# Optimization experiments

Measured on AMD Instinct MI355X. Metric: run time of the kernel, lower is better.

Reference implementation:

```python
import jax, jax.numpy as jnp
import numpy as np

# ---- maxflat pyramid filters (pfilters('maxflat')) ----
def _maxflat_filters():
    sqrt2 = np.sqrt(2.0)
    M1 = M2 = 1.0 / sqrt2
    k1 = 1.0 - sqrt2
    k2 = k3 = M1
    h_half = np.array([0.25 * k2 * k3, 0.5 * k2, 1.0 + 0.5 * k2 * k3]) * M1
    h = np.concatenate([h_half, h_half[:-1][::-1]]) * sqrt2          # len 5
    g_half = np.array([-0.125 * k1 * k2 * k3,
                       0.25 * k1 * k2,
                       -0.5 * k1 - 0.5 * k3 - 0.375 * k1 * k2 * k3,
                       1.0 + 0.5 * k1 * k2]) * M2
    g = np.concatenate([g_half, g_half[:-1][::-1]]) * sqrt2          # len 7
    return h.astype(np.float32), g.astype(np.float32)

# highpass from g, as in wfb2dec: h1 = -g * (-1)**(arange(1,L+1)-c)
def _wfb_filters():
    h, g = _maxflat_filters()
    len_h1 = len(g)                      # 7 (odd)
    c = int(np.floor((len_h1 + 1.0) / 2.0))   # 4
    h1 = (-g * (-1.0) ** (np.arange(1, len_h1 + 1) - c)).astype(np.float32)
    ext_h0 = int(np.floor(len(h) / 2.0))      # 2
    ext_h1 = len_h1 - c + 1                   # 4
    return h, h1, ext_h0, ext_h1

# periodic row filtering along last axis (torch rowfiltering: periodic pad +
# cross-correlation, which F.conv2d / lax conv both compute without flip)
def rowfilt(x, f, ext1):
    L = f.shape[0]
    ext2 = L - ext1 - 1
    W = x.shape[-1]
    xe = jnp.concatenate([x[..., -ext1:], x, x[..., :ext2]], axis=-1)
    y = f[0] * xe[..., 0:W]
    for k in range(1, L):                 # tiny fixed tap loop, fuses fine
        y = y + f[k] * xe[..., k:k + W]
    return y

def colfilt(x, f, ext1):
    return jnp.swapaxes(rowfilt(jnp.swapaxes(x, -1, -2), f, ext1), -1, -2)


def setup_inputs() -> dict:
    key = jax.random.key(0)
    x = jax.random.normal(key, (8, 3, 1024, 1024), dtype=jnp.float32)
    return {"x": x}


def reference(x):
    # Pycontourlet.batch_multi_channel_pdfbdec with pfilt='maxflat',
    # nlevs=[0] -> wfb2dec path: one level of separable wavelet FB with
    # periodic extension; returns [xLL, [xLH, xHL, xHH]] (stacked here).
    h_np, h1_np, e0, e1 = _wfb_filters()
    h = jnp.asarray(h_np)
    h1 = jnp.asarray(h1_np)

    x_L = rowfilt(x, h, e0)[..., ::2]          # [B,C,H,W/2]
    x_H = rowfilt(x, h1, e1)[..., ::2]

    x_LL = colfilt(x_L, h, e0)[..., ::2, :]    # [B,C,H/2,W/2]
    x_LH = colfilt(x_L, h1, e1)[..., ::2, :]
    x_HL = colfilt(x_H, h, e0)[..., ::2, :]
    x_HH = colfilt(x_H, h1, e1)[..., ::2, :]

    return jnp.stack([x_LL, x_LH, x_HL, x_HH])  # [4,B,C,H/2,W/2]
```

## Files before the change

kernel.cpp:

```cpp
#include <hip/hip_runtime.h>


constexpr int H = 1024, W = 1024;
constexpr int NIMG = 24;
constexpr int HOUT = 512, WOUT = 512;
constexpr int TO = 32;
constexpr int TI = 2 * TO + 6;

__global__ __launch_bounds__(256)
void wfb_kernel(const float* __restrict__ x, float* __restrict__ out) {
    __shared__ float s_in[TI][TI + 2];
    __shared__ float s_L[TI][TO + 1];
    __shared__ float s_H[TI][TO + 1];

    const float h0c[5] = {0.125f, 0.35355339059327373f, 1.25f,
                          0.35355339059327373f, 0.125f};
    const float h1c[7] = {0.025888347648318447f,  0.07322330470336313f,
                          -0.06878156646177083f, -0.8535533905932737f,
                          -0.06878156646177083f,  0.07322330470336313f,
                          0.025888347648318447f};

    const int tid = threadIdx.x;
    const int img = blockIdx.z;
    const int r0 = blockIdx.y * TO;
    const int c0 = blockIdx.x * TO;
    const float* __restrict__ xin = x + (size_t)img * H * W;

    const int rbase = 2 * r0 - 4;
    const int cbase = 2 * c0 - 4;
    for (int idx = tid; idx < TI * TI; idx += 256) {
        int r = idx / TI;
        int c = idx - r * TI;
        int gr = (rbase + r) & (H - 1);
        int gc = (cbase + c) & (W - 1);
        s_in[r][c] = xin[gr * W + gc];
    }
    __syncthreads();

    for (int idx = tid; idx < TI * TO; idx += 256) {
        int r = idx >> 5;
        int j = idx & 31;
        const float* row = &s_in[r][2 * j];
        float L  = h0c[0]*row[2] + h0c[1]*row[3] + h0c[2]*row[4]
                 + h0c[3]*row[5] + h0c[4]*row[6];
        float Hv = h1c[0]*row[0] + h1c[1]*row[1] + h1c[2]*row[2]
                 + h1c[3]*row[3] + h1c[4]*row[4] + h1c[5]*row[5]
                 + h1c[6]*row[6];
        s_L[r][j] = L;
        s_H[r][j] = Hv;
    }
    __syncthreads();

    constexpr size_t SB = (size_t)NIMG * HOUT * WOUT;
    float* __restrict__ o = out + (size_t)img * HOUT * WOUT;
    for (int idx = tid; idx < TO * TO; idx += 256) {
        int i = idx >> 5;
        int j = idx & 31;
        float LL = 0.f, LH = 0.f, HL = 0.f, HHv = 0.f;
        #pragma unroll
        for (int k = 0; k < 5; ++k) {
            LL += h0c[k] * s_L[2*i + 2 + k][j];
            HL += h0c[k] * s_H[2*i + 2 + k][j];
        }
        #pragma unroll
        for (int k = 0; k < 7; ++k) {
            LH  += h1c[k] * s_L[2*i + k][j];
            HHv += h1c[k] * s_H[2*i + k][j];
        }
        size_t off = (size_t)(r0 + i) * WOUT + (c0 + j);
        o[0 * SB + off] = LL;
        o[1 * SB + off] = LH;
        o[2 * SB + off] = HL;
        o[3 * SB + off] = HHv;
    }
}

extern "C" void kernel_launch(void* const* d_in, const int* in_sizes, int n_in,
                              void* d_out, int out_size, void* d_ws, size_t ws_size,
                              hipStream_t stream) {
    const float* x = (const float*)d_in[0];
    float* out = (float*)d_out;
    dim3 grid(WOUT / TO, HOUT / TO, NIMG);
    wfb_kernel<<<grid, dim3(256), 0, stream>>>(x, out);
}
```

Measured before the change: 187.3 us.

## Fuse row filtering into global load and vectorize column-stage stores

```diff
diff --git a/kernel.cpp b/kernel.cpp
--- a/kernel.cpp
+++ b/kernel.cpp
@@ -5,13 +5,13 @@
 constexpr int NIMG = 24;
 constexpr int HOUT = 512, WOUT = 512;
 constexpr int TO = 32;
-constexpr int TI = 2 * TO + 6;
+constexpr int RIN = 69;
+constexpr int PAD = 34;
 
 __global__ __launch_bounds__(256)
 void wfb_kernel(const float* __restrict__ x, float* __restrict__ out) {
-    __shared__ float s_in[TI][TI + 2];
-    __shared__ float s_L[TI][TO + 1];
-    __shared__ float s_H[TI][TO + 1];
+    __shared__ float s_L[RIN][PAD];
+    __shared__ float s_H[RIN][PAD];
 
     const float h0c[5] = {0.125f, 0.35355339059327373f, 1.25f,
                           0.35355339059327373f, 0.125f};
@@ -25,53 +25,54 @@
     const int r0 = blockIdx.y * TO;
     const int c0 = blockIdx.x * TO;
     const float* __restrict__ xin = x + (size_t)img * H * W;
-
     const int rbase = 2 * r0 - 4;
     const int cbase = 2 * c0 - 4;
-    for (int idx = tid; idx < TI * TI; idx += 256) {
-        int r = idx / TI;
-        int c = idx - r * TI;
+
+    for (int m = tid; m < RIN * TO; m += 256) {
+        int r = m >> 5;
+        int j = m & 31;
         int gr = (rbase + r) & (H - 1);
-        int gc = (cbase + c) & (W - 1);
-        s_in[r][c] = xin[gr * W + gc];
-    }
-    __syncthreads();
-
-    for (int idx = tid; idx < TI * TO; idx += 256) {
-        int r = idx >> 5;
-        int j = idx & 31;
-        const float* row = &s_in[r][2 * j];
-        float L  = h0c[0]*row[2] + h0c[1]*row[3] + h0c[2]*row[4]
-                 + h0c[3]*row[5] + h0c[4]*row[6];
-        float Hv = h1c[0]*row[0] + h1c[1]*row[1] + h1c[2]*row[2]
-                 + h1c[3]*row[3] + h1c[4]*row[4] + h1c[5]*row[5]
-                 + h1c[6]*row[6];
-        s_L[r][j] = L;
-        s_H[r][j] = Hv;
+        const float* __restrict__ rowp = xin + (size_t)gr * W;
+        int b = cbase + 2 * j;
+        float v0 = rowp[(b + 0) & (W - 1)];
+        float v1 = rowp[(b + 1) & (W - 1)];
+        float v2 = rowp[(b + 2) & (W - 1)];
+        float v3 = rowp[(b + 3) & (W - 1)];
+        float v4 = rowp[(b + 4) & (W - 1)];
+        float v5 = rowp[(b + 5) & (W - 1)];
+        float v6 = rowp[(b + 6) & (W - 1)];
+        s_L[r][j] = h0c[0]*v2 + h0c[1]*v3 + h0c[2]*v4 + h0c[3]*v5 + h0c[4]*v6;
+        s_H[r][j] = h1c[0]*v0 + h1c[1]*v1 + h1c[2]*v2 + h1c[3]*v3
+                  + h1c[4]*v4 + h1c[5]*v5 + h1c[6]*v6;
     }
     __syncthreads();
 
     constexpr size_t SB = (size_t)NIMG * HOUT * WOUT;
     float* __restrict__ o = out + (size_t)img * HOUT * WOUT;
-    for (int idx = tid; idx < TO * TO; idx += 256) {
-        int i = idx >> 5;
-        int j = idx & 31;
-        float LL = 0.f, LH = 0.f, HL = 0.f, HHv = 0.f;
+    for (int m = tid; m < TO * (TO / 2); m += 256) {
+        int i  = m >> 4;
+        int jj = (m & 15) * 2;
+        float LLx = 0.f, LLy = 0.f, HLx = 0.f, HLy = 0.f;
+        float LHx = 0.f, LHy = 0.f, HHx = 0.f, HHy = 0.f;
         #pragma unroll
         for (int k = 0; k < 5; ++k) {
-            LL += h0c[k] * s_L[2*i + 2 + k][j];
-            HL += h0c[k] * s_H[2*i + 2 + k][j];
+            float a0 = s_L[2*i + 2 + k][jj], a1 = s_L[2*i + 2 + k][jj + 1];
+            float b0 = s_H[2*i + 2 + k][jj], b1 = s_H[2*i + 2 + k][jj + 1];
+            LLx += h0c[k] * a0;  LLy += h0c[k] * a1;
+            HLx += h0c[k] * b0;  HLy += h0c[k] * b1;
         }
         #pragma unroll
         for (int k = 0; k < 7; ++k) {
-            LH  += h1c[k] * s_L[2*i + k][j];
-            HHv += h1c[k] * s_H[2*i + k][j];
+            float a0 = s_L[2*i + k][jj], a1 = s_L[2*i + k][jj + 1];
+            float b0 = s_H[2*i + k][jj], b1 = s_H[2*i + k][jj + 1];
+            LHx += h1c[k] * a0;  LHy += h1c[k] * a1;
+            HHx += h1c[k] * b0;  HHy += h1c[k] * b1;
         }
-        size_t off = (size_t)(r0 + i) * WOUT + (c0 + j);
-        o[0 * SB + off] = LL;
-        o[1 * SB + off] = LH;
-        o[2 * SB + off] = HL;
-        o[3 * SB + off] = HHv;
+        size_t off = (size_t)(r0 + i) * WOUT + (c0 + jj);
+        *(float2*)(o + 0 * SB + off) = make_float2(LLx, LLy);
+        *(float2*)(o + 1 * SB + off) = make_float2(LHx, LHy);
+        *(float2*)(o + 2 * SB + off) = make_float2(HLx, HLy);
+        *(float2*)(o + 3 * SB + off) = make_float2(HHx, HHy);
     }
 }
 
```

After: 207.2 us. 10.7% more time.

## Replace shared-memory tiles with register-streaming row sweep per wavefront

Applied to the files above, without the earlier changes.

```diff
diff --git a/kernel.cpp b/kernel.cpp
--- a/kernel.cpp
+++ b/kernel.cpp
@@ -4,15 +4,50 @@
 constexpr int H = 1024, W = 1024;
 constexpr int NIMG = 24;
 constexpr int HOUT = 512, WOUT = 512;
-constexpr int TO = 32;
-constexpr int TI = 2 * TO + 6;
+constexpr int CH = 16;
+constexpr int NSTRIP = 4;
+constexpr int NCHUNK = HOUT / CH;
+constexpr size_t SB = (size_t)NIMG * HOUT * WOUT;
+
+struct Raw { float4 v; float4 h4; float h1v; };
+
+__device__ __forceinline__ Raw load_row(const float* __restrict__ imgp,
+                                        int gr, int ci, int lane) {
+    Raw r;
+    const float* __restrict__ rowp = imgp + (size_t)gr * W;
+    r.v = *(const float4*)(rowp + ci + 4 * lane);
+    if (lane == 0)  r.h4  = *(const float4*)(rowp + ((ci - 4) & (W - 1)));
+    if (lane == 63) r.h1v = rowp[(ci + 256) & (W - 1)];
+    return r;
+}
+
+__device__ __forceinline__ void rowfilt(const Raw& r, int lane,
+                                        float& rLa, float& rHa,
+                                        float& rLb, float& rHb) {
+    const float h0c[5] = {0.125f, 0.35355339059327373f, 1.25f,
+                          0.35355339059327373f, 0.125f};
+    const float h1c[7] = {0.025888347648318447f,  0.07322330470336313f,
+                          -0.06878156646177083f, -0.8535533905932737f,
+                          -0.06878156646177083f,  0.07322330470336313f,
+                          0.025888347648318447f};
+    float4 vm1;
+    vm1.x = __shfl_up(r.v.x, 1);
+    vm1.y = __shfl_up(r.v.y, 1);
+    vm1.z = __shfl_up(r.v.z, 1);
+    vm1.w = __shfl_up(r.v.w, 1);
+    float vp1 = __shfl_down(r.v.x, 1);
+    if (lane == 0)  vm1 = r.h4;
+    if (lane == 63) vp1 = r.h1v;
+    rLa = h0c[0]*vm1.z + h0c[1]*vm1.w + h0c[2]*r.v.x + h0c[3]*r.v.y + h0c[4]*r.v.z;
+    rHa = h1c[0]*vm1.x + h1c[1]*vm1.y + h1c[2]*vm1.z + h1c[3]*vm1.w
+        + h1c[4]*r.v.x + h1c[5]*r.v.y + h1c[6]*r.v.z;
+    rLb = h0c[0]*r.v.x + h0c[1]*r.v.y + h0c[2]*r.v.z + h0c[3]*r.v.w + h0c[4]*vp1;
+    rHb = h1c[0]*vm1.z + h1c[1]*vm1.w + h1c[2]*r.v.x + h1c[3]*r.v.y
+        + h1c[4]*r.v.z + h1c[5]*r.v.w + h1c[6]*vp1;
+}
 
 __global__ __launch_bounds__(256)
 void wfb_kernel(const float* __restrict__ x, float* __restrict__ out) {
-    __shared__ float s_in[TI][TI + 2];
-    __shared__ float s_L[TI][TO + 1];
-    __shared__ float s_H[TI][TO + 1];
-
     const float h0c[5] = {0.125f, 0.35355339059327373f, 1.25f,
                           0.35355339059327373f, 0.125f};
     const float h1c[7] = {0.025888347648318447f,  0.07322330470336313f,
@@ -20,58 +55,75 @@
                           -0.06878156646177083f,  0.07322330470336313f,
                           0.025888347648318447f};
 
-    const int tid = threadIdx.x;
-    const int img = blockIdx.z;
-    const int r0 = blockIdx.y * TO;
-    const int c0 = blockIdx.x * TO;
+    const int tid  = threadIdx.x;
+    const int lane = tid & 63;
+    const int gwid = blockIdx.x * 4 + (tid >> 6);
+    const int img   = gwid >> 7;
+    const int rem   = gwid & 127;
+    const int chunk = rem >> 2;
+    const int strip = rem & 3;
+
+    const int i0 = chunk * CH;
+    const int ci = strip * 256;
+    const int oc = strip * 128 + 2 * lane;
+
     const float* __restrict__ xin = x + (size_t)img * H * W;
+    float* __restrict__ o = out + (size_t)img * HOUT * WOUT;
 
-    const int rbase = 2 * r0 - 4;
-    const int cbase = 2 * c0 - 4;
-    for (int idx = tid; idx < TI * TI; idx += 256) {
-        int r = idx / TI;
-        int c = idx - r * TI;
-        int gr = (rbase + r) & (H - 1);
-        int gc = (cbase + c) & (W - 1);
-        s_in[r][c] = xin[gr * W + gc];
+    float La0,La1,La2,La3,La4,La5, Ha0,Ha1,Ha2,Ha3,Ha4,Ha5;
+    float Lb0,Lb1,Lb2,Lb3,Lb4,Lb5, Hb0,Hb1,Hb2,Hb3,Hb4,Hb5;
+    {
+        Raw t0 = load_row(xin, (2*i0 - 4) & (H-1), ci, lane);
+        Raw t1 = load_row(xin, (2*i0 - 3) & (H-1), ci, lane);
+        Raw t2 = load_row(xin, (2*i0 - 2) & (H-1), ci, lane);
+        Raw t3 = load_row(xin, (2*i0 - 1) & (H-1), ci, lane);
+        Raw t4 = load_row(xin, (2*i0 + 0) & (H-1), ci, lane);
+        Raw t5 = load_row(xin, (2*i0 + 1) & (H-1), ci, lane);
+        rowfilt(t0, lane, La0, Ha0, Lb0, Hb0);
+        rowfilt(t1, lane, La1, Ha1, Lb1, Hb1);
+        rowfilt(t2, lane, La2, Ha2, Lb2, Hb2);
+        rowfilt(t3, lane, La3, Ha3, Lb3, Hb3);
+        rowfilt(t4, lane, La4, Ha4, Lb4, Hb4);
+        rowfilt(t5, lane, La5, Ha5, Lb5, Hb5);
     }
-    __syncthreads();
 
-    for (int idx = tid; idx < TI * TO; idx += 256) {
-        int r = idx >> 5;
-        int j = idx & 31;
-        const float* row = &s_in[r][2 * j];
-        float L  = h0c[0]*row[2] + h0c[1]*row[3] + h0c[2]*row[4]
-                 + h0c[3]*row[5] + h0c[4]*row[6];
-        float Hv = h1c[0]*row[0] + h1c[1]*row[1] + h1c[2]*row[2]
-                 + h1c[3]*row[3] + h1c[4]*row[4] + h1c[5]*row[5]
-                 + h1c[6]*row[6];
-        s_L[r][j] = L;
-        s_H[r][j] = Hv;
-    }
-    __syncthreads();
+    Raw ra = load_row(xin, (2*i0 + 2) & (H-1), ci, lane);
+    Raw rb = load_row(xin, (2*i0 + 3) & (H-1), ci, lane);
 
-    constexpr size_t SB = (size_t)NIMG * HOUT * WOUT;
-    float* __restrict__ o = out + (size_t)img * HOUT * WOUT;
-    for (int idx = tid; idx < TO * TO; idx += 256) {
-        int i = idx >> 5;
-        int j = idx & 31;
-        float LL = 0.f, LH = 0.f, HL = 0.f, HHv = 0.f;
-        #pragma unroll
-        for (int k = 0; k < 5; ++k) {
-            LL += h0c[k] * s_L[2*i + 2 + k][j];
-            HL += h0c[k] * s_H[2*i + 2 + k][j];
-        }
-        #pragma unroll
-        for (int k = 0; k < 7; ++k) {
-            LH  += h1c[k] * s_L[2*i + k][j];
-            HHv += h1c[k] * s_H[2*i + k][j];
-        }
-        size_t off = (size_t)(r0 + i) * WOUT + (c0 + j);
-        o[0 * SB + off] = LL;
-        o[1 * SB + off] = LH;
-        o[2 * SB + off] = HL;
-        o[3 * SB + off] = HHv;
+    for (int t = 0; t < CH; ++t) {
+        const int gi = i0 + t;
+        Raw na = load_row(xin, (2*gi + 4) & (H-1), ci, lane);
+        Raw nb = load_row(xin, (2*gi + 5) & (H-1), ci, lane);
+
+        float La6, Ha6, Lb6, Hb6;
+        rowfilt(ra, lane, La6, Ha6, Lb6, Hb6);
+
+        float LLa = h0c[0]*La2 + h0c[1]*La3 + h0c[2]*La4 + h0c[3]*La5 + h0c[4]*La6;
+        float HLa = h0c[0]*Ha2 + h0c[1]*Ha3 + h0c[2]*Ha4 + h0c[3]*Ha5 + h0c[4]*Ha6;
+        float LHa = h1c[0]*La0 + h1c[1]*La1 + h1c[2]*La2 + h1c[3]*La3
+                  + h1c[4]*La4 + h1c[5]*La5 + h1c[6]*La6;
+        float HHa = h1c[0]*Ha0 + h1c[1]*Ha1 + h1c[2]*Ha2 + h1c[3]*Ha3
+                  + h1c[4]*Ha4 + h1c[5]*Ha5 + h1c[6]*Ha6;
+        float LLb = h0c[0]*Lb2 + h0c[1]*Lb3 + h0c[2]*Lb4 + h0c[3]*Lb5 + h0c[4]*Lb6;
+        float HLb = h0c[0]*Hb2 + h0c[1]*Hb3 + h0c[2]*Hb4 + h0c[3]*Hb5 + h0c[4]*Hb6;
+        float LHb = h1c[0]*Lb0 + h1c[1]*Lb1 + h1c[2]*Lb2 + h1c[3]*Lb3
+                  + h1c[4]*Lb4 + h1c[5]*Lb5 + h1c[6]*Lb6;
+        float HHb = h1c[0]*Hb0 + h1c[1]*Hb1 + h1c[2]*Hb2 + h1c[3]*Hb3
+                  + h1c[4]*Hb4 + h1c[5]*Hb5 + h1c[6]*Hb6;
+
+        size_t off = (size_t)gi * WOUT + oc;
+        *(float2*)(o + 0 * SB + off) = make_float2(LLa, LLb);
+        *(float2*)(o + 1 * SB + off) = make_float2(LHa, LHb);
+        *(float2*)(o + 2 * SB + off) = make_float2(HLa, HLb);
+        *(float2*)(o + 3 * SB + off) = make_float2(HHa, HHb);
+
+        float nLa5, nHa5, nLb5, nHb5;
+        rowfilt(rb, lane, nLa5, nHa5, nLb5, nHb5);
+        La0 = La2; La1 = La3; La2 = La4; La3 = La5; La4 = La6; La5 = nLa5;
+        Ha0 = Ha2; Ha1 = Ha3; Ha2 = Ha4; Ha3 = Ha5; Ha4 = Ha6; Ha5 = nHa5;
+        Lb0 = Lb2; Lb1 = Lb3; Lb2 = Lb4; Lb3 = Lb5; Lb4 = Lb6; Lb5 = nLb5;
+        Hb0 = Hb2; Hb1 = Hb3; Hb2 = Hb4; Hb3 = Hb5; Hb4 = Hb6; Hb5 = nHb5;
+        ra = na; rb = nb;
     }
 }
 
@@ -80,6 +132,6 @@
                               hipStream_t stream) {
     const float* x = (const float*)d_in[0];
     float* out = (float*)d_out;
-    dim3 grid(WOUT / TO, HOUT / TO, NIMG);
-    wfb_kernel<<<grid, dim3(256), 0, stream>>>(x, out);
+    int nblocks = NIMG * NCHUNK * NSTRIP / 4;
+    wfb_kernel<<<nblocks, dim3(256), 0, stream>>>(x, out);
 }
```

Measured after the change: 183.7 us. No clear change (-1.9%).
